# Optimization experiments

Hardware: AMD Instinct MI355X
Metric: run time of the kernel (lower is better)

Reference implementation:

```python
import jax, jax.numpy as jnp
import numpy as np

N = 20000
E = 320000
IN_F = 128
HEADS = 8
OUT_F = 32
NEG_SLOPE = 0.2


def setup_inputs() -> dict:
    key = jax.random.key(0)
    k = jax.random.split(key, 8)
    x = jax.random.normal(k[0], (N, IN_F), dtype=jnp.float32)
    edge_index = jax.random.randint(k[1], (2, E), 0, N, dtype=jnp.int32)
    # Linear weights stored torch-style: [out, in]
    scale = 1.0 / np.sqrt(IN_F)
    W = jax.random.normal(k[2], (HEADS * OUT_F, IN_F), dtype=jnp.float32) * scale
    W1 = jax.random.normal(k[3], (HEADS * OUT_F, IN_F), dtype=jnp.float32) * scale
    W2 = jax.random.normal(k[4], (HEADS * OUT_F, IN_F), dtype=jnp.float32) * scale
    att = jax.random.normal(k[5], (1, HEADS, OUT_F), dtype=jnp.float32) * 0.1
    bias = jnp.zeros((HEADS * OUT_F,), dtype=jnp.float32)
    return {"x": x, "edge_index": edge_index, "W": W, "W1": W1, "W2": W2,
            "att": att, "bias": bias}


def reference(x, edge_index, W, W1, W2, att, bias):
    n, heads, out_f = x.shape[0], att.shape[1], att.shape[2]
    src, dst = edge_index[0], edge_index[1]

    # Node projections: [N, H, F]
    h_src = (x @ W1.T).reshape(n, heads, out_f)
    h_dst = (x @ W2.T).reshape(n, heads, out_f)
    values = (x @ W.T).reshape(n, heads, out_f)

    # Edge-wise GATv2 logits: a^T LeakyReLU(W1 h_i + W2 h_j)  -> [E, H]
    att_input = jax.nn.leaky_relu(h_src[src] + h_dst[dst], negative_slope=NEG_SLOPE)
    logits = jnp.einsum('ehf,hf->eh', att_input, att[0])

    # Segment softmax over incoming edges of each dst node (stable).
    seg_max = jax.ops.segment_max(logits, dst, num_segments=n)  # [N, H]
    exp_l = jnp.exp(logits - seg_max[dst])
    denom = jax.ops.segment_sum(exp_l, dst, num_segments=n)     # [N, H]
    weights = exp_l / denom[dst]                                # [E, H]

    # Weighted aggregation of source values into dst nodes.
    weighted = weights[:, :, None] * values[src]                # [E, H, F]
    out = jax.ops.segment_sum(weighted, dst, num_segments=n)    # [N, H, F]

    out = out.reshape(n, heads * out_f) + bias
    return out
```

## Files before the change

### kernel.cpp

```cpp
#include <hip/hip_runtime.h>
#include <math.h>

#define NN 20000
#define EE 320000
#define KF 128
#define HO 256
#define CAP 96

typedef __attribute__((ext_vector_type(8))) short short8;
typedef __attribute__((ext_vector_type(4))) float f32x4;

static __device__ __forceinline__ unsigned short f2bf(float f) {
    union { float f; unsigned u; } v; v.f = f;
    unsigned u = v.u;
    u += 0x7fffu + ((u >> 16) & 1u);
    return (unsigned short)(u >> 16);
}
static __device__ __forceinline__ float bf2f(unsigned short b) {
    union { unsigned u; float f; } v; v.u = ((unsigned)b) << 16;
    return v.f;
}

__global__ __launch_bounds__(256) void prep_kernel(
    const float* __restrict__ x, const float* __restrict__ W0,
    const float* __restrict__ W1, const float* __restrict__ W2,
    unsigned short* __restrict__ xb, unsigned short* __restrict__ wb,
    int* __restrict__ cursor)
{
    const int b = blockIdx.x;
    const int t = threadIdx.x;
    if (b < 96) {
        const int m = b >> 5;
        const float* __restrict__ Wm = (m == 0) ? W0 : (m == 1) ? W1 : W2;
        int idx = (b & 31) * 1024 + t * 4;
        float4 v = *(const float4*)(Wm + idx);
        ushort4 o;
        o.x = f2bf(v.x); o.y = f2bf(v.y); o.z = f2bf(v.z); o.w = f2bf(v.w);
        *(ushort4*)(wb + (size_t)m * 32768 + idx) = o;
    } else if (b < 2596) {
        size_t i = (size_t)(b - 96) * 1024 + t * 4;
        float4 v = *(const float4*)(x + i);
        ushort4 o;
        o.x = f2bf(v.x); o.y = f2bf(v.y); o.z = f2bf(v.z); o.w = f2bf(v.w);
        *(ushort4*)(xb + i) = o;
    } else {
        int i = (b - 2596) * 256 + t;
        if (i < NN) cursor[i] = 0;
    }
}

__global__ void scatter_kernel(const int* __restrict__ ei, int* __restrict__ cursor,
                               int* __restrict__ csr_src) {
    int e = blockIdx.x * blockDim.x + threadIdx.x;
    if (e < EE) {
        int s = ei[e];
        int d = ei[EE + e];
        int pos = atomicAdd(&cursor[d], 1);
        if (pos < CAP) csr_src[d * CAP + pos] = s;
    }
}

__global__ __launch_bounds__(256, 4) void proj_kernel(
    const unsigned short* __restrict__ xb, const unsigned short* __restrict__ wb,
    unsigned short* __restrict__ hv, unsigned short* __restrict__ hdst)
{
    const int m = blockIdx.y;
    const unsigned short* __restrict__ Wm = wb + (size_t)m * 32768;
    unsigned short* __restrict__ dst = (m == 0) ? (hv + 256) : (m == 1) ? hv : hdst;
    const int stride = (m == 2) ? 256 : 512;

    const int w    = threadIdx.x >> 6;
    const int lane = threadIdx.x & 63;
    const int lr   = lane & 15;
    const int q    = lane >> 4;
    const int cb   = w * 64;

    short8 Bf[4][4];
#pragma unroll
    for (int nt = 0; nt < 4; ++nt)
#pragma unroll
        for (int ks = 0; ks < 4; ++ks)
            Bf[nt][ks] = *(const short8*)(Wm + (size_t)(cb + nt * 16 + lr) * KF + ks * 32 + q * 8);

    const int rb = blockIdx.x * 64;

#pragma unroll
    for (int it = 0; it < 4; ++it) {
        const int r0 = rb + it * 16;

        short8 Af[4];
        const int arow = r0 + lr;
#pragma unroll
        for (int ks = 0; ks < 4; ++ks) {
            Af[ks] = (short8){0,0,0,0,0,0,0,0};
            if (arow < NN)
                Af[ks] = *(const short8*)(xb + (size_t)arow * KF + ks * 32 + q * 8);
        }

        f32x4 acc[4];
#pragma unroll
        for (int nt = 0; nt < 4; ++nt) acc[nt] = (f32x4){0.f, 0.f, 0.f, 0.f};

#pragma unroll
        for (int ks = 0; ks < 4; ++ks)
#pragma unroll
            for (int nt = 0; nt < 4; ++nt)
                acc[nt] = __builtin_amdgcn_mfma_f32_16x16x32_bf16(Af[ks], Bf[nt][ks], acc[nt], 0, 0, 0);

#pragma unroll
        for (int nt = 0; nt < 4; ++nt) {
#pragma unroll
            for (int r = 0; r < 4; ++r) {
                const int row = r0 + q * 4 + r;
                if (row < NN)
                    dst[(size_t)row * stride + cb + nt * 16 + lr] = f2bf(acc[nt][r]);
            }
        }
    }
}

__global__ __launch_bounds__(128) void gat_kernel(
    const unsigned short* __restrict__ hv, const unsigned short* __restrict__ hdst,
    const float* __restrict__ att, const float* __restrict__ bias,
    const int* __restrict__ cursor, const int* __restrict__ csr_src,
    float* __restrict__ out)
{
    const int w    = threadIdx.x >> 6;
    const int d    = blockIdx.x * 2 + w;
    const int lane = threadIdx.x & 63;
    const int col  = lane * 4;

    const float4 a4 = *(const float4*)(att + col);
    const float4 b4 = *(const float4*)(bias + col);
    const ushort4 hd4 = *(const ushort4*)(hdst + (size_t)d * HO + col);
    const float hd0 = bf2f(hd4.x), hd1 = bf2f(hd4.y), hd2 = bf2f(hd4.z), hd3 = bf2f(hd4.w);

    int deg = cursor[d];
    if (deg > CAP) deg = CAP;

    int sreg = (lane < deg) ? csr_src[d * CAP + lane] : 0;

    float l = 0.f;
    float o0 = 0.f, o1 = 0.f, o2 = 0.f, o3 = 0.f;

#define EDGE_CALC(HV, VV)                                                     \
    {                                                                         \
        float z0 = bf2f(HV.x) + hd0, z1 = bf2f(HV.y) + hd1;                   \
        float z2 = bf2f(HV.z) + hd2, z3 = bf2f(HV.w) + hd3;                   \
        z0 = fmaxf(z0, 0.2f * z0); z1 = fmaxf(z1, 0.2f * z1);                 \
        z2 = fmaxf(z2, 0.2f * z2); z3 = fmaxf(z3, 0.2f * z3);                 \
        float p = fmaf(a4.x, z0, a4.y * z1) + fmaf(a4.z, z2, a4.w * z3);      \
        p += __shfl_xor(p, 1); p += __shfl_xor(p, 2); p += __shfl_xor(p, 4);  \
        const float e = __expf(p);                                            \
        l += e;                                                               \
        o0 = fmaf(e, bf2f(VV.x), o0);                                         \
        o1 = fmaf(e, bf2f(VV.y), o1);                                         \
        o2 = fmaf(e, bf2f(VV.z), o2);                                         \
        o3 = fmaf(e, bf2f(VV.w), o3);                                         \
    }

    const int nfast = (deg < 64) ? deg : 64;
    int i = 0;
    for (; i + 4 <= nfast; i += 4) {
        const int s0 = __shfl(sreg, i);
        const int s1 = __shfl(sreg, i + 1);
        const int s2 = __shfl(sreg, i + 2);
        const int s3 = __shfl(sreg, i + 3);
        const unsigned short* p0 = hv + (size_t)s0 * 512 + col;
        const unsigned short* p1 = hv + (size_t)s1 * 512 + col;
        const unsigned short* p2 = hv + (size_t)s2 * 512 + col;
        const unsigned short* p3 = hv + (size_t)s3 * 512 + col;
        const ushort4 hv0 = *(const ushort4*)p0;
        const ushort4 vv0 = *(const ushort4*)(p0 + 256);
        const ushort4 hv1 = *(const ushort4*)p1;
        const ushort4 vv1 = *(const ushort4*)(p1 + 256);
        const ushort4 hv2 = *(const ushort4*)p2;
        const ushort4 vv2 = *(const ushort4*)(p2 + 256);
        const ushort4 hv3 = *(const ushort4*)p3;
        const ushort4 vv3 = *(const ushort4*)(p3 + 256);
        EDGE_CALC(hv0, vv0);
        EDGE_CALC(hv1, vv1);
        EDGE_CALC(hv2, vv2);
        EDGE_CALC(hv3, vv3);
    }
    for (; i < nfast; ++i) {
        const int s0 = __shfl(sreg, i);
        const unsigned short* p0 = hv + (size_t)s0 * 512 + col;
        const ushort4 hv0 = *(const ushort4*)p0;
        const ushort4 vv0 = *(const ushort4*)(p0 + 256);
        EDGE_CALC(hv0, vv0);
    }
    for (int j = 64; j < deg; ++j) {
        const int s0 = csr_src[d * CAP + j];
        const unsigned short* p0 = hv + (size_t)s0 * 512 + col;
        const ushort4 hv0 = *(const ushort4*)p0;
        const ushort4 vv0 = *(const ushort4*)(p0 + 256);
        EDGE_CALC(hv0, vv0);
    }
#undef EDGE_CALC

    const float inv = (deg > 0) ? 1.f / l : 0.f;
    float4 res;
    res.x = o0 * inv + b4.x;
    res.y = o1 * inv + b4.y;
    res.z = o2 * inv + b4.z;
    res.w = o3 * inv + b4.w;
    *(float4*)(out + (size_t)d * HO + col) = res;
}

extern "C" void kernel_launch(void* const* d_in, const int* in_sizes, int n_in,
                              void* d_out, int out_size, void* d_ws, size_t ws_size,
                              hipStream_t stream) {
    const float* x    = (const float*)d_in[0];
    const int*   ei   = (const int*)d_in[1];
    const float* W0   = (const float*)d_in[2];
    const float* W1   = (const float*)d_in[3];
    const float* W2   = (const float*)d_in[4];
    const float* att  = (const float*)d_in[5];
    const float* bias = (const float*)d_in[6];
    float* out = (float*)d_out;

    char* p = (char*)d_ws;
    unsigned short* hv   = (unsigned short*)p; p += (size_t)NN * 512 * 2;
    unsigned short* hdst = (unsigned short*)p; p += (size_t)NN * HO * 2;
    unsigned short* xb   = (unsigned short*)p; p += (size_t)NN * KF * 2;
    unsigned short* wb   = (unsigned short*)p; p += (size_t)3 * 32768 * 2;
    int* cursor  = (int*)p; p += (size_t)NN * sizeof(int);
    int* csr_src = (int*)p; p += (size_t)NN * CAP * sizeof(int);

    prep_kernel<<<2675, 256, 0, stream>>>(x, W0, W1, W2, xb, wb, cursor);
    scatter_kernel<<<(EE + 255) / 256, 256, 0, stream>>>(ei, cursor, csr_src);
    proj_kernel<<<dim3(313, 3), 256, 0, stream>>>(xb, wb, hv, hdst);
    gat_kernel<<<NN / 2, 128, 0, stream>>>(hv, hdst, att, bias, cursor, csr_src, out);
}
```

Measured before the change: 161.1 us.

## Fuse scatter into projection kernel and compute attention logits in packed fp16

Merges the CSR scatter and projection GEMM into one launch, with the block index deciding which task each block runs. The attention-side projections h_src and h_dst are now stored as fp16. LeakyReLU plus the dot product is rewritten as 0.6*a·z + 0.4*a·|z|, evaluated with packed fdot2, which cuts ALU work per edge. The edge loop is unified with masked tail handling instead of a separate remainder loop, at the cost of fp16 rounding and range limits on the logits.

Measured after the change: 157.3 us. -2.3%, faster.

```diff
diff --git a/kernel.cpp b/kernel.cpp
--- a/kernel.cpp
+++ b/kernel.cpp
@@ -9,6 +9,7 @@
 
 typedef __attribute__((ext_vector_type(8))) short short8;
 typedef __attribute__((ext_vector_type(4))) float f32x4;
+typedef __attribute__((ext_vector_type(2))) _Float16 half2_t;
 
 static __device__ __forceinline__ unsigned short f2bf(float f) {
     union { float f; unsigned u; } v; v.f = f;
@@ -16,9 +17,16 @@
     u += 0x7fffu + ((u >> 16) & 1u);
     return (unsigned short)(u >> 16);
 }
-static __device__ __forceinline__ float bf2f(unsigned short b) {
-    union { unsigned u; float f; } v; v.u = ((unsigned)b) << 16;
-    return v.f;
+static __device__ __forceinline__ unsigned short f2h(float f) {
+    _Float16 h = (_Float16)f;
+    return __builtin_bit_cast(unsigned short, h);
+}
+static __device__ __forceinline__ float dot2f(half2_t a, half2_t b, float c) {
+#if __has_builtin(__builtin_amdgcn_fdot2)
+    return __builtin_amdgcn_fdot2(a, b, c, false);
+#else
+    return c + (float)a[0] * (float)b[0] + (float)a[1] * (float)b[1];
+#endif
 }
 
 __global__ __launch_bounds__(256) void prep_kernel(
@@ -49,22 +57,25 @@
     }
 }
 
-__global__ void scatter_kernel(const int* __restrict__ ei, int* __restrict__ cursor,
-                               int* __restrict__ csr_src) {
-    int e = blockIdx.x * blockDim.x + threadIdx.x;
-    if (e < EE) {
-        int s = ei[e];
-        int d = ei[EE + e];
-        int pos = atomicAdd(&cursor[d], 1);
-        if (pos < CAP) csr_src[d * CAP + pos] = s;
-    }
-}
-
-__global__ __launch_bounds__(256, 4) void proj_kernel(
+__global__ __launch_bounds__(256, 4) void mid_kernel(
     const unsigned short* __restrict__ xb, const unsigned short* __restrict__ wb,
-    unsigned short* __restrict__ hv, unsigned short* __restrict__ hdst)
+    unsigned short* __restrict__ hv, unsigned short* __restrict__ hdst,
+    const int* __restrict__ ei, int* __restrict__ cursor, int* __restrict__ csr_src)
 {
-    const int m = blockIdx.y;
+    const int bid = blockIdx.x;
+    if (bid < 1250) {
+        const int e = bid * 256 + threadIdx.x;
+        if (e < EE) {
+            int s = ei[e];
+            int d = ei[EE + e];
+            int pos = atomicAdd(&cursor[d], 1);
+            if (pos < CAP) csr_src[d * CAP + pos] = s;
+        }
+        return;
+    }
+    const int pb = bid - 1250;
+    const int m  = (pb < 313) ? 0 : (pb < 626) ? 1 : 2;
+    const int bx = pb - m * 313;
     const unsigned short* __restrict__ Wm = wb + (size_t)m * 32768;
     unsigned short* __restrict__ dst = (m == 0) ? (hv + 256) : (m == 1) ? hv : hdst;
     const int stride = (m == 2) ? 256 : 512;
@@ -82,7 +93,7 @@
         for (int ks = 0; ks < 4; ++ks)
             Bf[nt][ks] = *(const short8*)(Wm + (size_t)(cb + nt * 16 + lr) * KF + ks * 32 + q * 8);
 
-    const int rb = blockIdx.x * 64;
+    const int rb = bx * 64;
 
 #pragma unroll
     for (int it = 0; it < 4; ++it) {
@@ -112,8 +123,11 @@
 #pragma unroll
             for (int r = 0; r < 4; ++r) {
                 const int row = r0 + q * 4 + r;
-                if (row < NN)
-                    dst[(size_t)row * stride + cb + nt * 16 + lr] = f2bf(acc[nt][r]);
+                if (row < NN) {
+                    const float val = acc[nt][r];
+                    dst[(size_t)row * stride + cb + nt * 16 + lr] =
+                        (m == 0) ? f2bf(val) : f2h(val);
+                }
             }
         }
     }
@@ -130,10 +144,16 @@
     const int lane = threadIdx.x & 63;
     const int col  = lane * 4;
 
-    const float4 a4 = *(const float4*)(att + col);
+    const float4 av = *(const float4*)(att + col);
+    const half2_t a6_01 = { (_Float16)(0.6f * av.x), (_Float16)(0.6f * av.y) };
+    const half2_t a6_23 = { (_Float16)(0.6f * av.z), (_Float16)(0.6f * av.w) };
+    const half2_t a4_01 = { (_Float16)(0.4f * av.x), (_Float16)(0.4f * av.y) };
+    const half2_t a4_23 = { (_Float16)(0.4f * av.z), (_Float16)(0.4f * av.w) };
     const float4 b4 = *(const float4*)(bias + col);
-    const ushort4 hd4 = *(const ushort4*)(hdst + (size_t)d * HO + col);
-    const float hd0 = bf2f(hd4.x), hd1 = bf2f(hd4.y), hd2 = bf2f(hd4.z), hd3 = bf2f(hd4.w);
+
+    const uint2 hdb = *(const uint2*)(hdst + (size_t)d * HO + col);
+    const half2_t hd01 = __builtin_bit_cast(half2_t, hdb.x);
+    const half2_t hd23 = __builtin_bit_cast(half2_t, hdb.y);
 
     int deg = cursor[d];
     if (deg > CAP) deg = CAP;
@@ -143,68 +163,71 @@
     float l = 0.f;
     float o0 = 0.f, o1 = 0.f, o2 = 0.f, o3 = 0.f;
 
-#define EDGE_CALC(HV, VV)                                                     \
+#define EDGE_CALC(HS, VV, VMUL)                                               \
     {                                                                         \
-        float z0 = bf2f(HV.x) + hd0, z1 = bf2f(HV.y) + hd1;                   \
-        float z2 = bf2f(HV.z) + hd2, z3 = bf2f(HV.w) + hd3;                   \
-        z0 = fmaxf(z0, 0.2f * z0); z1 = fmaxf(z1, 0.2f * z1);                 \
-        z2 = fmaxf(z2, 0.2f * z2); z3 = fmaxf(z3, 0.2f * z3);                 \
-        float p = fmaf(a4.x, z0, a4.y * z1) + fmaf(a4.z, z2, a4.w * z3);      \
+        half2_t z01 = __builtin_bit_cast(half2_t, HS.x) + hd01;               \
+        half2_t z23 = __builtin_bit_cast(half2_t, HS.y) + hd23;               \
+        unsigned zu01 = __builtin_bit_cast(unsigned, z01) & 0x7FFF7FFFu;      \
+        unsigned zu23 = __builtin_bit_cast(unsigned, z23) & 0x7FFF7FFFu;      \
+        float p = dot2f(a6_01, z01,                                           \
+                  dot2f(a6_23, z23,                                           \
+                  dot2f(a4_01, __builtin_bit_cast(half2_t, zu01),             \
+                  dot2f(a4_23, __builtin_bit_cast(half2_t, zu23), 0.f))));    \
         p += __shfl_xor(p, 1); p += __shfl_xor(p, 2); p += __shfl_xor(p, 4);  \
-        const float e = __expf(p);                                            \
+        const float e = __expf(p) * (VMUL);                                   \
         l += e;                                                               \
-        o0 = fmaf(e, bf2f(VV.x), o0);                                         \
-        o1 = fmaf(e, bf2f(VV.y), o1);                                         \
-        o2 = fmaf(e, bf2f(VV.z), o2);                                         \
-        o3 = fmaf(e, bf2f(VV.w), o3);                                         \
-    }
-
-    const int nfast = (deg < 64) ? deg : 64;
-    int i = 0;
-    for (; i + 4 <= nfast; i += 4) {
+        const float v0 = __builtin_bit_cast(float, VV.x << 16);              \
+        const float v1 = __builtin_bit_cast(float, VV.x & 0xFFFF0000u);      \
+        const float v2 = __builtin_bit_cast(float, VV.y << 16);              \
+        const float v3 = __builtin_bit_cast(float, VV.y & 0xFFFF0000u);      \
+        o0 = fmaf(e, v0, o0); o1 = fmaf(e, v1, o1);                           \
+        o2 = fmaf(e, v2, o2); o3 = fmaf(e, v3, o3);                           \
+    }
+
+    const int ng = (deg < 64) ? deg : 64;
+    for (int i = 0; i < ng; i += 4) {
+        const int j1 = (i + 1 < ng) ? i + 1 : ng - 1;
+        const int j2 = (i + 2 < ng) ? i + 2 : ng - 1;
+        const int j3 = (i + 3 < ng) ? i + 3 : ng - 1;
+        const float m1 = (i + 1 < ng) ? 1.f : 0.f;
+        const float m2 = (i + 2 < ng) ? 1.f : 0.f;
+        const float m3 = (i + 3 < ng) ? 1.f : 0.f;
         const int s0 = __shfl(sreg, i);
-        const int s1 = __shfl(sreg, i + 1);
-        const int s2 = __shfl(sreg, i + 2);
-        const int s3 = __shfl(sreg, i + 3);
+        const int s1 = __shfl(sreg, j1);
+        const int s2 = __shfl(sreg, j2);
+        const int s3 = __shfl(sreg, j3);
         const unsigned short* p0 = hv + (size_t)s0 * 512 + col;
         const unsigned short* p1 = hv + (size_t)s1 * 512 + col;
         const unsigned short* p2 = hv + (size_t)s2 * 512 + col;
         const unsigned short* p3 = hv + (size_t)s3 * 512 + col;
-        const ushort4 hv0 = *(const ushort4*)p0;
-        const ushort4 vv0 = *(const ushort4*)(p0 + 256);
-        const ushort4 hv1 = *(const ushort4*)p1;
-        const ushort4 vv1 = *(const ushort4*)(p1 + 256);
-        const ushort4 hv2 = *(const ushort4*)p2;
-        const ushort4 vv2 = *(const ushort4*)(p2 + 256);
-        const ushort4 hv3 = *(const ushort4*)p3;
-        const ushort4 vv3 = *(const ushort4*)(p3 + 256);
-        EDGE_CALC(hv0, vv0);
-        EDGE_CALC(hv1, vv1);
-        EDGE_CALC(hv2, vv2);
-        EDGE_CALC(hv3, vv3);
-    }
-    for (; i < nfast; ++i) {
-        const int s0 = __shfl(sreg, i);
-        const unsigned short* p0 = hv + (size_t)s0 * 512 + col;
-        const ushort4 hv0 = *(const ushort4*)p0;
-        const ushort4 vv0 = *(const ushort4*)(p0 + 256);
-        EDGE_CALC(hv0, vv0);
+        const uint2 hs0 = *(const uint2*)p0;
+        const uint2 vv0 = *(const uint2*)(p0 + 256);
+        const uint2 hs1 = *(const uint2*)p1;
+        const uint2 vv1 = *(const uint2*)(p1 + 256);
+        const uint2 hs2 = *(const uint2*)p2;
+        const uint2 vv2 = *(const uint2*)(p2 + 256);
+        const uint2 hs3 = *(const uint2*)p3;
+        const uint2 vv3 = *(const uint2*)(p3 + 256);
+        EDGE_CALC(hs0, vv0, 1.f);
+        EDGE_CALC(hs1, vv1, m1);
+        EDGE_CALC(hs2, vv2, m2);
+        EDGE_CALC(hs3, vv3, m3);
     }
     for (int j = 64; j < deg; ++j) {
         const int s0 = csr_src[d * CAP + j];
         const unsigned short* p0 = hv + (size_t)s0 * 512 + col;
-        const ushort4 hv0 = *(const ushort4*)p0;
-        const ushort4 vv0 = *(const ushort4*)(p0 + 256);
-        EDGE_CALC(hv0, vv0);
+        const uint2 hs0 = *(const uint2*)p0;
+        const uint2 vv0 = *(const uint2*)(p0 + 256);
+        EDGE_CALC(hs0, vv0, 1.f);
     }
 #undef EDGE_CALC
 
     const float inv = (deg > 0) ? 1.f / l : 0.f;
     float4 res;
-    res.x = o0 * inv + b4.x;
-    res.y = o1 * inv + b4.y;
-    res.z = o2 * inv + b4.z;
-    res.w = o3 * inv + b4.w;
+    res.x = fmaf(o0, inv, b4.x);
+    res.y = fmaf(o1, inv, b4.y);
+    res.z = fmaf(o2, inv, b4.z);
+    res.w = fmaf(o3, inv, b4.w);
     *(float4*)(out + (size_t)d * HO + col) = res;
 }
 
@@ -229,7 +252,6 @@
     int* csr_src = (int*)p; p += (size_t)NN * CAP * sizeof(int);
 
     prep_kernel<<<2675, 256, 0, stream>>>(x, W0, W1, W2, xb, wb, cursor);
-    scatter_kernel<<<(EE + 255) / 256, 256, 0, stream>>>(ei, cursor, csr_src);
-    proj_kernel<<<dim3(313, 3), 256, 0, stream>>>(xb, wb, hv, hdst);
+    mid_kernel<<<2189, 256, 0, stream>>>(xb, wb, hv, hdst, ei, cursor, csr_src);
     gat_kernel<<<NN / 2, 128, 0, stream>>>(hv, hdst, att, bias, cursor, csr_src, out);
 }
```
